# Kernel optimization log

Hardware: AMD Instinct MI355X
Metric: run time of the kernel (lower is better)

The kernel has to match this reference:

```python
import jax, jax.numpy as jnp
import numpy as np


def setup_inputs() -> dict:
    key = jax.random.key(0)
    k1, k2, k3 = jax.random.split(key, 3)
    B, C, H, W = 32, 2048, 32, 32
    S = H * W  # spatial_size, must equal conv kernel size
    x = jax.random.normal(k1, (B, C, H, W), dtype=jnp.float32)
    # depthwise Conv1d weight [C, 1, S] and bias [C]
    weight = jax.random.normal(k2, (C, 1, S), dtype=jnp.float32) * (1.0 / np.sqrt(S))
    bias = jax.random.normal(k3, (C,), dtype=jnp.float32) * 0.01
    return {"x": x, "weight": weight, "bias": bias}


def reference(x, weight, bias):
    B, C, H, W = x.shape
    S = H * W
    x = x.reshape(B, C, S)
    # topk(k=S) == full sort descending per channel
    x_sorted = jnp.flip(jnp.sort(x, axis=-1), axis=-1)  # [B, C, S]
    # depthwise conv1d with kernel spanning S -> per-channel dot product, out len 1
    w = weight[:, 0, :]  # [C, S]
    out = jnp.einsum("bcs,cs->bc", x_sorted, w) + bias  # [B, C]
    return out[:, :, None]  # [B, C, 1] (flatten=False)
```

## Files before the change

### kernel.cpp

```cpp
#include <hip/hip_runtime.h>


#define C_DIM 2048
#define S_DIM 1024

__global__ __launch_bounds__(256) void rankpool_wave_kernel(
    const float* __restrict__ x, const float* __restrict__ w,
    const float* __restrict__ bias, float* __restrict__ out) {
  const int t    = threadIdx.x;
  const int wid  = t >> 6;
  const int lane = t & 63;
  const int bc   = (blockIdx.x << 2) | wid;
  const int c    = bc & (C_DIM - 1);

  float r[16];
  {
    const float4* x4 = (const float4*)(x + (size_t)bc * S_DIM);
    #pragma unroll
    for (int q2 = 0; q2 < 4; ++q2) {
      const float4 v = x4[(q2 << 6) + lane];
      r[4 * q2 + 0] = v.x; r[4 * q2 + 1] = v.y;
      r[4 * q2 + 2] = v.z; r[4 * q2 + 3] = v.w;
    }
  }

  #pragma unroll
  for (int k = 2; k <= S_DIM; k <<= 1) {
    #pragma unroll
    for (int j = k >> 1; j > 0; j >>= 1) {
      if (j >= 16) {
        const int  xl      = j >> 4;
        const bool takemax = ((lane & xl) == 0) == ((lane & (k >> 4)) == 0);
        #pragma unroll
        for (int q = 0; q < 16; ++q) {
          const float p = __shfl_xor(r[q], xl, 64);
          r[q] = takemax ? fmaxf(r[q], p) : fminf(r[q], p);
        }
      } else {
        #pragma unroll
        for (int q = 0; q < 16; ++q) {
          const int l = q ^ j;
          if (l > q) {
            const bool desc = (k >= 16) ? ((lane & (k >> 4)) == 0)
                                        : ((q & k) == 0);
            const float a = r[q], b = r[l];
            const float hi = fmaxf(a, b), lo = fminf(a, b);
            r[q] = desc ? hi : lo;
            r[l] = desc ? lo : hi;
          }
        }
      }
    }
  }

  const float4* w4 = (const float4*)(w + (size_t)c * S_DIM);
  float acc = 0.f;
  #pragma unroll
  for (int q2 = 0; q2 < 4; ++q2) {
    const float4 wv = w4[(lane << 2) + q2];
    acc += r[4 * q2 + 0] * wv.x + r[4 * q2 + 1] * wv.y +
           r[4 * q2 + 2] * wv.z + r[4 * q2 + 3] * wv.w;
  }

  #pragma unroll
  for (int off = 32; off > 0; off >>= 1)
    acc += __shfl_down(acc, off, 64);
  if (lane == 0) out[bc] = acc + bias[c];
}

extern "C" void kernel_launch(void* const* d_in, const int* in_sizes, int n_in,
                              void* d_out, int out_size, void* d_ws, size_t ws_size,
                              hipStream_t stream) {
  const float* x    = (const float*)d_in[0];
  const float* w    = (const float*)d_in[1];
  const float* bias = (const float*)d_in[2];
  float* out        = (float*)d_out;

  rankpool_wave_kernel<<<(32 * C_DIM) / 4, 256, 0, stream>>>(x, w, bias, out);
}
```

Before: 521.3 us.

## Replace bitonic cross-lane shuffles with DPP swaps and sign-flip direction trick

Reworks the cross-lane stages of the per-wave bitonic sort. The first three in-register stages stay as before. The remaining stages replace per-element direction selects with a sign-bit flip of whole registers, so every local merge and cross-lane step always runs in one direction. Lane exchanges at distances 1, 2 and 8 use DPP update instructions instead of ds_bpermute-based shuffles. This is meant to cut LDS-permute traffic and select instructions, but it relies on the sign-flip and DPP control encodings being correct for ordering (NaN/−0 handling is also affected).

```diff
diff --git a/kernel.cpp b/kernel.cpp
--- a/kernel.cpp
+++ b/kernel.cpp
@@ -4,7 +4,57 @@
 #define C_DIM 2048
 #define S_DIM 1024
 
-__global__ __launch_bounds__(256) void rankpool_wave_kernel(
+__device__ __forceinline__ float fxor(float v, unsigned m) {
+  return __int_as_float(__float_as_int(v) ^ (int)m);
+}
+
+template <int CTRL>
+__device__ __forceinline__ float dpp_swap(float v) {
+  return __int_as_float(__builtin_amdgcn_update_dpp(
+      0, __float_as_int(v), CTRL, 0xF, 0xF, false));
+}
+
+template <int JL>
+__device__ __forceinline__ void cross_step(float (&r)[16], int lane) {
+  float p[16];
+  #pragma unroll
+  for (int q = 0; q < 16; ++q) {
+    if      (JL == 1) p[q] = dpp_swap<0xB1>(r[q]);
+    else if (JL == 2) p[q] = dpp_swap<0x4E>(r[q]);
+    else if (JL == 8) p[q] = dpp_swap<0x128>(r[q]);
+    else              p[q] = __shfl_xor(r[q], JL, 64);
+  }
+  if ((lane & JL) == 0) {
+    #pragma unroll
+    for (int q = 0; q < 16; ++q) r[q] = fmaxf(r[q], p[q]);
+  } else {
+    #pragma unroll
+    for (int q = 0; q < 16; ++q) r[q] = fminf(r[q], p[q]);
+  }
+}
+
+__device__ __forceinline__ void local_merge16(float (&r)[16]) {
+  #pragma unroll
+  for (int j = 8; j >= 1; j >>= 1) {
+    #pragma unroll
+    for (int q = 0; q < 16; ++q) {
+      const int l = q ^ j;
+      if (l > q) {
+        const float hi = fmaxf(r[q], r[l]);
+        const float lo = fminf(r[q], r[l]);
+        r[q] = hi; r[l] = lo;
+      }
+    }
+  }
+}
+
+__device__ __forceinline__ void flip_all(float (&r)[16], unsigned bit) {
+  const unsigned m = bit << 31;
+  #pragma unroll
+  for (int q = 0; q < 16; ++q) r[q] = fxor(r[q], m);
+}
+
+__global__ __launch_bounds__(256) void rankpool_dpp_kernel(
     const float* __restrict__ x, const float* __restrict__ w,
     const float* __restrict__ bias, float* __restrict__ out) {
   const int t    = threadIdx.x;
@@ -25,33 +75,47 @@
   }
 
   #pragma unroll
-  for (int k = 2; k <= S_DIM; k <<= 1) {
+  for (int k = 2; k <= 8; k <<= 1) {
     #pragma unroll
-    for (int j = k >> 1; j > 0; j >>= 1) {
-      if (j >= 16) {
-        const int  xl      = j >> 4;
-        const bool takemax = ((lane & xl) == 0) == ((lane & (k >> 4)) == 0);
-        #pragma unroll
-        for (int q = 0; q < 16; ++q) {
-          const float p = __shfl_xor(r[q], xl, 64);
-          r[q] = takemax ? fmaxf(r[q], p) : fminf(r[q], p);
-        }
-      } else {
-        #pragma unroll
-        for (int q = 0; q < 16; ++q) {
-          const int l = q ^ j;
-          if (l > q) {
-            const bool desc = (k >= 16) ? ((lane & (k >> 4)) == 0)
-                                        : ((q & k) == 0);
-            const float a = r[q], b = r[l];
-            const float hi = fmaxf(a, b), lo = fminf(a, b);
-            r[q] = desc ? hi : lo;
-            r[l] = desc ? lo : hi;
-          }
+    for (int j = k >> 1; j >= 1; j >>= 1) {
+      #pragma unroll
+      for (int q = 0; q < 16; ++q) {
+        const int l = q ^ j;
+        if (l > q) {
+          const bool desc = ((q & k) == 0);
+          const float hi = fmaxf(r[q], r[l]);
+          const float lo = fminf(r[q], r[l]);
+          r[q] = desc ? hi : lo;
+          r[l] = desc ? lo : hi;
         }
       }
     }
   }
+
+  flip_all(r, lane & 1u);
+
+  local_merge16(r);
+  flip_all(r, ((lane >> 0) ^ (lane >> 1)) & 1u);
+  cross_step<1>(r, lane);
+  local_merge16(r);
+  flip_all(r, ((lane >> 1) ^ (lane >> 2)) & 1u);
+  cross_step<2>(r, lane); cross_step<1>(r, lane);
+  local_merge16(r);
+  flip_all(r, ((lane >> 2) ^ (lane >> 3)) & 1u);
+  cross_step<4>(r, lane); cross_step<2>(r, lane); cross_step<1>(r, lane);
+  local_merge16(r);
+  flip_all(r, ((lane >> 3) ^ (lane >> 4)) & 1u);
+  cross_step<8>(r, lane); cross_step<4>(r, lane); cross_step<2>(r, lane);
+  cross_step<1>(r, lane);
+  local_merge16(r);
+  flip_all(r, ((lane >> 4) ^ (lane >> 5)) & 1u);
+  cross_step<16>(r, lane); cross_step<8>(r, lane); cross_step<4>(r, lane);
+  cross_step<2>(r, lane);  cross_step<1>(r, lane);
+  local_merge16(r);
+  flip_all(r, ((lane >> 5) ^ (lane >> 6)) & 1u);
+  cross_step<32>(r, lane); cross_step<16>(r, lane); cross_step<8>(r, lane);
+  cross_step<4>(r, lane);  cross_step<2>(r, lane);  cross_step<1>(r, lane);
+  local_merge16(r);
 
   const float4* w4 = (const float4*)(w + (size_t)c * S_DIM);
   float acc = 0.f;
@@ -76,5 +140,5 @@
   const float* bias = (const float*)d_in[2];
   float* out        = (float*)d_out;
 
-  rankpool_wave_kernel<<<(32 * C_DIM) / 4, 256, 0, stream>>>(x, w, bias, out);
+  rankpool_dpp_kernel<<<(32 * C_DIM) / 4, 256, 0, stream>>>(x, w, bias, out);
 }
```

New measurement: 512.2 us. No clear change (-1.7%).

## Rewrite bitonic sort with sign-flip trick and DPP/swizzle cross-lane exchanges

Applied to the files above, without the earlier changes.

Restructures the per-wave bitonic sort so each cross-lane compare-exchange becomes a single fmax against a negated partner, using sign-bit XOR flips to encode direction instead of per-lane select logic. Cross-lane exchanges use DPP row operations and ds_swizzle where possible instead of generic shuffles (bpermute), and the final reduction uses the same primitives. Intra-register merges are reorganized into a fixed descending merge16 after flips. This cuts VALU work and LDS-path shuffle latency, at the cost of subtle correctness reliance on sign-flip symmetry and DPP control encodings.

```diff
diff --git a/kernel.cpp b/kernel.cpp
--- a/kernel.cpp
+++ b/kernel.cpp
@@ -4,14 +4,67 @@
 #define C_DIM 2048
 #define S_DIM 1024
 
-__global__ __launch_bounds__(256) void rankpool_wave_kernel(
+template <int CTRL>
+__device__ __forceinline__ float dppf(float v) {
+  return __int_as_float(__builtin_amdgcn_update_dpp(
+      0, __float_as_int(v), CTRL, 0xF, 0xF, false));
+}
+template <int PAT>
+__device__ __forceinline__ float swzf(float v) {
+  return __int_as_float(__builtin_amdgcn_ds_swizzle(__float_as_int(v), PAT));
+}
+__device__ __forceinline__ float bperm(int addr, float v) {
+  return __int_as_float(__builtin_amdgcn_ds_bpermute(addr, __float_as_int(v)));
+}
+
+template <int JL>
+__device__ __forceinline__ void cross(float (&r)[16], int addr32) {
+  float p[16];
+  #pragma unroll
+  for (int q = 0; q < 16; ++q) {
+    if      (JL == 1)  p[q] = dppf<0xB1>(r[q]);
+    else if (JL == 2)  p[q] = dppf<0x4E>(r[q]);
+    else if (JL == 4)  p[q] = swzf<0x101F>(r[q]);
+    else if (JL == 8)  p[q] = dppf<0x128>(r[q]);
+    else if (JL == 16) p[q] = swzf<0x401F>(r[q]);
+    else               p[q] = bperm(addr32, r[q]);
+  }
+  #pragma unroll
+  for (int q = 0; q < 16; ++q) r[q] = fmaxf(r[q], -p[q]);
+}
+
+__device__ __forceinline__ void merge16(float (&r)[16]) {
+  #pragma unroll
+  for (int j = 8; j >= 1; j >>= 1) {
+    #pragma unroll
+    for (int q = 0; q < 16; ++q) {
+      const int l = q ^ j;
+      if (l > q) {
+        const float hi = fmaxf(r[q], r[l]);
+        const float lo = fminf(r[q], r[l]);
+        r[q] = hi; r[l] = lo;
+      }
+    }
+  }
+}
+
+__device__ __forceinline__ void flip(float (&r)[16], unsigned m) {
+  #pragma unroll
+  for (int q = 0; q < 16; ++q)
+    r[q] = __int_as_float(__float_as_int(r[q]) ^ (int)m);
+}
+
+__global__ __launch_bounds__(256) void rankpool_signspace_kernel(
     const float* __restrict__ x, const float* __restrict__ w,
     const float* __restrict__ bias, float* __restrict__ out) {
-  const int t    = threadIdx.x;
-  const int wid  = t >> 6;
-  const int lane = t & 63;
-  const int bc   = (blockIdx.x << 2) | wid;
-  const int c    = bc & (C_DIM - 1);
+  const int t      = threadIdx.x;
+  const int lane   = t & 63;
+  const int bc     = (blockIdx.x << 2) | (t >> 6);
+  const int c      = bc & (C_DIM - 1);
+  const int addr32 = (lane ^ 32) << 2;
+  const unsigned L = (unsigned)lane;
+  #define MB(b)      ((L << (31 - (b))) & 0x80000000u)
+  #define MX(bi, bj) (((L << (31-(bi))) ^ (L << (31-(bj)))) & 0x80000000u)
 
   float r[16];
   {
@@ -19,53 +72,109 @@
     #pragma unroll
     for (int q2 = 0; q2 < 4; ++q2) {
       const float4 v = x4[(q2 << 6) + lane];
-      r[4 * q2 + 0] = v.x; r[4 * q2 + 1] = v.y;
-      r[4 * q2 + 2] = v.z; r[4 * q2 + 3] = v.w;
+      r[4*q2+0] = v.x; r[4*q2+1] = v.y; r[4*q2+2] = v.z; r[4*q2+3] = v.w;
     }
   }
 
   #pragma unroll
-  for (int k = 2; k <= S_DIM; k <<= 1) {
+  for (int k = 2; k <= 8; k <<= 1) {
     #pragma unroll
-    for (int j = k >> 1; j > 0; j >>= 1) {
-      if (j >= 16) {
-        const int  xl      = j >> 4;
-        const bool takemax = ((lane & xl) == 0) == ((lane & (k >> 4)) == 0);
-        #pragma unroll
-        for (int q = 0; q < 16; ++q) {
-          const float p = __shfl_xor(r[q], xl, 64);
-          r[q] = takemax ? fmaxf(r[q], p) : fminf(r[q], p);
-        }
-      } else {
-        #pragma unroll
-        for (int q = 0; q < 16; ++q) {
-          const int l = q ^ j;
-          if (l > q) {
-            const bool desc = (k >= 16) ? ((lane & (k >> 4)) == 0)
-                                        : ((q & k) == 0);
-            const float a = r[q], b = r[l];
-            const float hi = fmaxf(a, b), lo = fminf(a, b);
-            r[q] = desc ? hi : lo;
-            r[l] = desc ? lo : hi;
-          }
+    for (int j = k >> 1; j >= 1; j >>= 1) {
+      #pragma unroll
+      for (int q = 0; q < 16; ++q) {
+        const int l = q ^ j;
+        if (l > q) {
+          const bool desc = ((q & k) == 0);
+          const float hi = fmaxf(r[q], r[l]);
+          const float lo = fminf(r[q], r[l]);
+          r[q] = desc ? hi : lo;
+          r[l] = desc ? lo : hi;
         }
       }
     }
   }
+
+  flip(r, MB(0));
+  merge16(r);
+
+  flip(r, MB(1));
+  cross<1>(r, addr32);
+  flip(r, MB(0));
+  merge16(r);
+
+  flip(r, MB(2));
+  cross<2>(r, addr32);
+  flip(r, MX(1, 0));
+  cross<1>(r, addr32);
+  flip(r, MB(0));
+  merge16(r);
+
+  flip(r, MB(3));
+  cross<4>(r, addr32);
+  flip(r, MX(2, 1));
+  cross<2>(r, addr32);
+  flip(r, MX(1, 0));
+  cross<1>(r, addr32);
+  flip(r, MB(0));
+  merge16(r);
+
+  flip(r, MB(4));
+  cross<8>(r, addr32);
+  flip(r, MX(3, 2));
+  cross<4>(r, addr32);
+  flip(r, MX(2, 1));
+  cross<2>(r, addr32);
+  flip(r, MX(1, 0));
+  cross<1>(r, addr32);
+  flip(r, MB(0));
+  merge16(r);
+
+  flip(r, MB(5));
+  cross<16>(r, addr32);
+  flip(r, MX(4, 3));
+  cross<8>(r, addr32);
+  flip(r, MX(3, 2));
+  cross<4>(r, addr32);
+  flip(r, MX(2, 1));
+  cross<2>(r, addr32);
+  flip(r, MX(1, 0));
+  cross<1>(r, addr32);
+  flip(r, MB(0));
+  merge16(r);
+
+  cross<32>(r, addr32);
+  flip(r, MX(5, 4));
+  cross<16>(r, addr32);
+  flip(r, MX(4, 3));
+  cross<8>(r, addr32);
+  flip(r, MX(3, 2));
+  cross<4>(r, addr32);
+  flip(r, MX(2, 1));
+  cross<2>(r, addr32);
+  flip(r, MX(1, 0));
+  cross<1>(r, addr32);
+  flip(r, MB(0));
+  merge16(r);
 
   const float4* w4 = (const float4*)(w + (size_t)c * S_DIM);
   float acc = 0.f;
   #pragma unroll
   for (int q2 = 0; q2 < 4; ++q2) {
     const float4 wv = w4[(lane << 2) + q2];
-    acc += r[4 * q2 + 0] * wv.x + r[4 * q2 + 1] * wv.y +
-           r[4 * q2 + 2] * wv.z + r[4 * q2 + 3] * wv.w;
+    acc += r[4*q2+0] * wv.x + r[4*q2+1] * wv.y +
+           r[4*q2+2] * wv.z + r[4*q2+3] * wv.w;
   }
 
-  #pragma unroll
-  for (int off = 32; off > 0; off >>= 1)
-    acc += __shfl_down(acc, off, 64);
+  acc += dppf<0xB1>(acc);
+  acc += dppf<0x4E>(acc);
+  acc += swzf<0x101F>(acc);
+  acc += dppf<0x128>(acc);
+  acc += swzf<0x401F>(acc);
+  acc += bperm(addr32, acc);
   if (lane == 0) out[bc] = acc + bias[c];
+
+  #undef MB
+  #undef MX
 }
 
 extern "C" void kernel_launch(void* const* d_in, const int* in_sizes, int n_in,
@@ -76,5 +185,5 @@
   const float* bias = (const float*)d_in[2];
   float* out        = (float*)d_out;
 
-  rankpool_wave_kernel<<<(32 * C_DIM) / 4, 256, 0, stream>>>(x, w, bias, out);
+  rankpool_signspace_kernel<<<(32 * C_DIM) / 4, 256, 0, stream>>>(x, w, bias, out);
 }
```

Result: faster. 504.5 us (-3.2%).
